# Kernel tuning notes

Hardware: AMD Instinct MI355X
Metric: run time of the kernel (lower is better)

Reference implementation:

```python
import jax, jax.numpy as jnp
import numpy as np

B, S, H, F, E, TOP_K = 2, 1024, 2048, 1408, 8, 2
SHARED_F = 2 * F  # moe_intermediate_size * n_shared_experts


def setup_inputs() -> dict:
    key = jax.random.key(0)
    ks = jax.random.split(key, 8)
    s = 0.02  # init scale for weights
    return {
        "hidden_states": jax.random.normal(ks[0], (B, S, H), jnp.float32),
        "gate_weight": jax.random.normal(ks[1], (E, H), jnp.float32) * s,
        "gate_proj": jax.random.normal(ks[2], (E, H, F), jnp.float32) * s,
        "up_proj": jax.random.normal(ks[3], (E, H, F), jnp.float32) * s,
        "down_proj": jax.random.normal(ks[4], (E, F, H), jnp.float32) * s,
        "shared_gate": jax.random.normal(ks[5], (H, SHARED_F), jnp.float32) * s,
        "shared_up": jax.random.normal(ks[6], (H, SHARED_F), jnp.float32) * s,
        "shared_down": jax.random.normal(ks[7], (SHARED_F, H), jnp.float32) * s,
    }


def reference(hidden_states, gate_weight, gate_proj, up_proj, down_proj,
              shared_gate, shared_up, shared_down):
    orig_shape = hidden_states.shape
    x = hidden_states.reshape(-1, orig_shape[-1])  # [T, H]
    T = x.shape[0]

    # MoEGate: softmax scores, top-k routing (no renorm)
    scores = jax.nn.softmax(x @ gate_weight.T, axis=-1)  # [T, E]
    topk_w, topk_idx = jax.lax.top_k(scores, TOP_K)      # [T, K]
    # dense combine weights: zero except selected experts
    combine = jnp.zeros_like(scores).at[jnp.arange(T)[:, None], topk_idx].set(topk_w)  # [T, E]

    # FusedSigmaMLP on all experts (math equal to sort/pad/grouped-GEMM/scatter-add path)
    gate_h = jnp.einsum('td,edf->etf', x, gate_proj)     # [E, T, F]
    up_h = jnp.einsum('td,edf->etf', x, up_proj)          # [E, T, F]
    expert_out = jnp.einsum('etf,efd->etd', jax.nn.silu(gate_h) * up_h, down_proj)  # [E, T, H]
    y = jnp.einsum('etd,te->td', expert_out, combine)     # weighted combine

    # shared experts (SigmaMLP with intermediate = moe_intermediate * n_shared)
    shared = (jax.nn.silu(x @ shared_gate) * (x @ shared_up)) @ shared_down
    return (y + shared).reshape(orig_shape)
```

## Files before the change

### kernel.cpp

```cpp
#include <hip/hip_runtime.h>
#include <hip/hip_bf16.h>

constexpr int T_ = 2048;
constexpr int H_ = 2048;
constexpr int F_ = 1408;
constexpr int E_ = 8;
constexpr int SF_ = 2816;

typedef __bf16 bf16;
typedef bf16 bf16x8 __attribute__((ext_vector_type(8)));
typedef float f32x4 __attribute__((ext_vector_type(4)));

#define DEVI __device__ __forceinline__

DEVI void async16(const void* g, void* l) {
    __builtin_amdgcn_global_load_lds(
        (const __attribute__((address_space(1))) unsigned int*)g,
        (__attribute__((address_space(3))) unsigned int*)l, 16, 0, 0);
}

__global__ void transpose_cvt(const float* __restrict__ src, bf16* __restrict__ dst,
                              int R, int C) {
    int z = blockIdx.z;
    src += (size_t)z * R * C;
    dst += (size_t)z * R * C;
    __shared__ float tile[32][33];
    int tx = threadIdx.x, ty = threadIdx.y;
    int c0 = blockIdx.x * 32, r0 = blockIdx.y * 32;
#pragma unroll
    for (int i = 0; i < 4; i++)
        tile[ty + i * 8][tx] = src[(size_t)(r0 + ty + i * 8) * C + c0 + tx];
    __syncthreads();
#pragma unroll
    for (int i = 0; i < 4; i++)
        dst[(size_t)(c0 + ty + i * 8) * R + r0 + tx] = (bf16)tile[tx][ty + i * 8];
}

__global__ void convert_x(const float* __restrict__ x, bf16* __restrict__ xb) {
    int i = (blockIdx.x * 256 + threadIdx.x) * 8;
    float4 a = *(const float4*)(x + i);
    float4 b = *(const float4*)(x + i + 4);
    bf16x8 v;
    v[0] = (bf16)a.x; v[1] = (bf16)a.y; v[2] = (bf16)a.z; v[3] = (bf16)a.w;
    v[4] = (bf16)b.x; v[5] = (bf16)b.y; v[6] = (bf16)b.z; v[7] = (bf16)b.w;
    *(bf16x8*)(xb + i) = v;
}

__global__ void gate_route(const float* __restrict__ x, const float* __restrict__ gw,
                           int* __restrict__ cnt, int* __restrict__ list,
                           float* __restrict__ wlist) {
    int t = blockIdx.x;
    int tid = threadIdx.x;
    float p[E_];
#pragma unroll
    for (int e = 0; e < E_; e++) p[e] = 0.f;
    const float* xr = x + (size_t)t * H_;
    for (int h = tid; h < H_; h += 256) {
        float xv = xr[h];
#pragma unroll
        for (int e = 0; e < E_; e++) p[e] += xv * gw[e * H_ + h];
    }
#pragma unroll
    for (int e = 0; e < E_; e++)
#pragma unroll
        for (int off = 32; off > 0; off >>= 1) p[e] += __shfl_down(p[e], off, 64);
    __shared__ float wred[4][E_];
    int lane = tid & 63, wid = tid >> 6;
    if (lane == 0)
#pragma unroll
        for (int e = 0; e < E_; e++) wred[wid][e] = p[e];
    __syncthreads();
    if (tid == 0) {
        float l[E_];
#pragma unroll
        for (int e = 0; e < E_; e++) l[e] = wred[0][e] + wred[1][e] + wred[2][e] + wred[3][e];
        float mx = l[0];
#pragma unroll
        for (int e = 1; e < E_; e++) mx = fmaxf(mx, l[e]);
        float sc[E_], s = 0.f;
#pragma unroll
        for (int e = 0; e < E_; e++) { sc[e] = __expf(l[e] - mx); s += sc[e]; }
#pragma unroll
        for (int e = 0; e < E_; e++) sc[e] /= s;
        int i1 = 0;
#pragma unroll
        for (int e = 1; e < E_; e++) if (sc[e] > sc[i1]) i1 = e;
        int i2 = (i1 == 0) ? 1 : 0;
#pragma unroll
        for (int e = 0; e < E_; e++) if (e != i1 && sc[e] > sc[i2]) i2 = e;
        int p1 = atomicAdd(&cnt[i1], 1);
        list[i1 * T_ + p1] = t; wlist[i1 * T_ + p1] = sc[i1];
        int p2 = atomicAdd(&cnt[i2], 1);
        list[i2 * T_ + p2] = t; wlist[i2 * T_ + p2] = sc[i2];
    }
}

__global__ void gather_rows(const bf16* __restrict__ xb, const int* __restrict__ cnt,
                            const int* __restrict__ list, bf16* __restrict__ xA) {
    int i = blockIdx.x, e = blockIdx.y;
    if (i >= cnt[e]) return;
    int t = list[e * T_ + i];
    const float4* s = (const float4*)(xb + (size_t)t * H_);
    float4* d = (float4*)(xA + ((size_t)e * T_ + i) * H_);
    d[threadIdx.x] = s[threadIdx.x];
}

__global__ void gemm_dual(const bf16* __restrict__ A, const bf16* __restrict__ Bg,
                          const bf16* __restrict__ Bu, bf16* __restrict__ Cact,
                          const int* __restrict__ cntPtr, int Mfull, int K, int N,
                          long sAe, long sBe, long sCe) {
    int e = blockIdx.z;
    A += (size_t)e * sAe; Bg += (size_t)e * sBe; Bu += (size_t)e * sBe;
    Cact += (size_t)e * sCe;
    int M = cntPtr ? cntPtr[e] : Mfull;
    int row0 = blockIdx.y * 128;
    if (row0 >= M) return;
    int col0 = blockIdx.x * 64;

    __shared__ __align__(16) bf16 As[128 * 64];
    __shared__ __align__(16) bf16 Bgs[64 * 64];
    __shared__ __align__(16) bf16 Bus[64 * 64];

    int tid = threadIdx.x, lane = tid & 63, wid = tid >> 6;
    int wm = (wid >> 1) * 64, wn = (wid & 1) * 32;
    int lm = lane & 15, lq = lane >> 4;

    f32x4 accg[4][2] = {};
    f32x4 accu[4][2] = {};

    int nkt = K >> 6;
    for (int kt = 0; kt < nkt; kt++) {
        int k0 = kt * 64;
#pragma unroll
        for (int j = 0; j < 4; j++) {
            int L = j * 256 + tid;
            int m = L >> 3, cp = L & 7, c = cp ^ (m & 7);
            int gr = row0 + m; if (gr >= M) gr = M - 1;
            async16(A + (size_t)gr * K + k0 + c * 8, (void*)(As + L * 8));
        }
#pragma unroll
        for (int j = 0; j < 2; j++) {
            int L = j * 256 + tid;
            int n = L >> 3, cp = L & 7, c = cp ^ (n & 7);
            async16(Bg + (size_t)(col0 + n) * K + k0 + c * 8, (void*)(Bgs + L * 8));
            async16(Bu + (size_t)(col0 + n) * K + k0 + c * 8, (void*)(Bus + L * 8));
        }
        __syncthreads();
#pragma unroll
        for (int kk = 0; kk < 2; kk++) {
            bf16x8 af[4], bgf[2], buf_[2];
            int cc = kk * 4 + lq;
#pragma unroll
            for (int mi = 0; mi < 4; mi++) {
                int r = wm + mi * 16 + lm;
                af[mi] = *(const bf16x8*)(As + r * 64 + ((cc ^ (r & 7)) * 8));
            }
#pragma unroll
            for (int ni = 0; ni < 2; ni++) {
                int r = wn + ni * 16 + lm;
                bgf[ni]  = *(const bf16x8*)(Bgs + r * 64 + ((cc ^ (r & 7)) * 8));
                buf_[ni] = *(const bf16x8*)(Bus + r * 64 + ((cc ^ (r & 7)) * 8));
            }
#pragma unroll
            for (int mi = 0; mi < 4; mi++)
#pragma unroll
                for (int ni = 0; ni < 2; ni++) {
                    accg[mi][ni] = __builtin_amdgcn_mfma_f32_16x16x32_bf16(af[mi], bgf[ni], accg[mi][ni], 0, 0, 0);
                    accu[mi][ni] = __builtin_amdgcn_mfma_f32_16x16x32_bf16(af[mi], buf_[ni], accu[mi][ni], 0, 0, 0);
                }
        }
        __syncthreads();
    }
#pragma unroll
    for (int mi = 0; mi < 4; mi++)
#pragma unroll
        for (int r = 0; r < 4; r++) {
            int gr = row0 + wm + mi * 16 + lq * 4 + r;
            if (gr >= M) continue;
#pragma unroll
            for (int ni = 0; ni < 2; ni++) {
                int gc = col0 + wn + ni * 16 + lm;
                float g = accg[mi][ni][r], u = accu[mi][ni][r];
                float act = g / (1.f + __expf(-g)) * u;
                Cact[(size_t)gr * N + gc] = (bf16)act;
            }
        }
}

__global__ void gemm_single(const bf16* __restrict__ A, const bf16* __restrict__ Bt,
                            float* __restrict__ Out, const int* __restrict__ cntPtr,
                            int Mfull, int K, int N, const int* __restrict__ list,
                            const float* __restrict__ wlist, long sAe, long sBe) {
    int e = blockIdx.z;
    A += (size_t)e * sAe; Bt += (size_t)e * sBe;
    const int* lst = list ? list + (size_t)e * T_ : nullptr;
    const float* wl = wlist ? wlist + (size_t)e * T_ : nullptr;
    int M = cntPtr ? cntPtr[e] : Mfull;
    int row0 = blockIdx.y * 128;
    if (row0 >= M) return;
    int col0 = blockIdx.x * 128;

    __shared__ __align__(16) bf16 As[128 * 64];
    __shared__ __align__(16) bf16 Bs[128 * 64];

    int tid = threadIdx.x, lane = tid & 63, wid = tid >> 6;
    int wm = (wid >> 1) * 64, wn = (wid & 1) * 64;
    int lm = lane & 15, lq = lane >> 4;

    f32x4 acc[4][4] = {};
    int nkt = K >> 6;
    for (int kt = 0; kt < nkt; kt++) {
        int k0 = kt * 64;
#pragma unroll
        for (int j = 0; j < 4; j++) {
            int L = j * 256 + tid;
            int m = L >> 3, cp = L & 7, c = cp ^ (m & 7);
            int gr = row0 + m; if (gr >= M) gr = M - 1;
            async16(A + (size_t)gr * K + k0 + c * 8, (void*)(As + L * 8));
            async16(Bt + (size_t)(col0 + m) * K + k0 + c * 8, (void*)(Bs + L * 8));
        }
        __syncthreads();
#pragma unroll
        for (int kk = 0; kk < 2; kk++) {
            bf16x8 af[4], bfr[4];
            int cc = kk * 4 + lq;
#pragma unroll
            for (int i = 0; i < 4; i++) {
                int ra = wm + i * 16 + lm;
                af[i] = *(const bf16x8*)(As + ra * 64 + ((cc ^ (ra & 7)) * 8));
                int rb = wn + i * 16 + lm;
                bfr[i] = *(const bf16x8*)(Bs + rb * 64 + ((cc ^ (rb & 7)) * 8));
            }
#pragma unroll
            for (int mi = 0; mi < 4; mi++)
#pragma unroll
                for (int ni = 0; ni < 4; ni++)
                    acc[mi][ni] = __builtin_amdgcn_mfma_f32_16x16x32_bf16(af[mi], bfr[ni], acc[mi][ni], 0, 0, 0);
        }
        __syncthreads();
    }
#pragma unroll
    for (int mi = 0; mi < 4; mi++)
#pragma unroll
        for (int r = 0; r < 4; r++) {
            int cr = row0 + wm + mi * 16 + lq * 4 + r;
            if (cr >= M) continue;
            if (lst) {
                int t = lst[cr];
                float w = wl[cr];
#pragma unroll
                for (int ni = 0; ni < 4; ni++) {
                    int gc = col0 + wn + ni * 16 + lm;
                    atomicAdd(&Out[(size_t)t * N + gc], w * acc[mi][ni][r]);
                }
            } else {
#pragma unroll
                for (int ni = 0; ni < 4; ni++) {
                    int gc = col0 + wn + ni * 16 + lm;
                    Out[(size_t)cr * N + gc] = acc[mi][ni][r];
                }
            }
        }
}

extern "C" void kernel_launch(void* const* d_in, const int* in_sizes, int n_in,
                              void* d_out, int out_size, void* d_ws, size_t ws_size,
                              hipStream_t stream) {
    const float* x     = (const float*)d_in[0];
    const float* gw    = (const float*)d_in[1];
    const float* gproj = (const float*)d_in[2];
    const float* uproj = (const float*)d_in[3];
    const float* dproj = (const float*)d_in[4];
    const float* sg    = (const float*)d_in[5];
    const float* su    = (const float*)d_in[6];
    const float* sd    = (const float*)d_in[7];
    float* out = (float*)d_out;

    char* w = (char*)d_ws;
    size_t off = 0;
    auto alloc = [&](size_t bytes) { void* p = w + off; off += (bytes + 255) & ~(size_t)255; return p; };
    bf16* wg_t   = (bf16*)alloc((size_t)E_ * F_ * H_ * 2);
    bf16* wu_t   = (bf16*)alloc((size_t)E_ * F_ * H_ * 2);
    bf16* wd_t   = (bf16*)alloc((size_t)E_ * H_ * F_ * 2);
    bf16* sg_t   = (bf16*)alloc((size_t)SF_ * H_ * 2);
    bf16* su_t   = (bf16*)alloc((size_t)SF_ * H_ * 2);
    bf16* sd_t   = (bf16*)alloc((size_t)H_ * SF_ * 2);
    bf16* xb     = (bf16*)alloc((size_t)T_ * H_ * 2);
    bf16* xA     = (bf16*)alloc((size_t)E_ * T_ * H_ * 2);
    bf16* act    = (bf16*)alloc((size_t)E_ * T_ * F_ * 2);
    bf16* act_sh = (bf16*)alloc((size_t)T_ * SF_ * 2);
    int*  cnt    = (int*)alloc(256);
    int*  list   = (int*)alloc((size_t)E_ * T_ * 4);
    float* wlist = (float*)alloc((size_t)E_ * T_ * 4);
    (void)ws_size; (void)in_sizes; (void)n_in; (void)out_size;

    hipMemsetAsync(cnt, 0, 256, stream);

    dim3 tb(32, 8);
    transpose_cvt<<<dim3(F_ / 32, H_ / 32, E_), tb, 0, stream>>>(gproj, wg_t, H_, F_);
    transpose_cvt<<<dim3(F_ / 32, H_ / 32, E_), tb, 0, stream>>>(uproj, wu_t, H_, F_);
    transpose_cvt<<<dim3(H_ / 32, F_ / 32, E_), tb, 0, stream>>>(dproj, wd_t, F_, H_);
    transpose_cvt<<<dim3(SF_ / 32, H_ / 32, 1), tb, 0, stream>>>(sg, sg_t, H_, SF_);
    transpose_cvt<<<dim3(SF_ / 32, H_ / 32, 1), tb, 0, stream>>>(su, su_t, H_, SF_);
    transpose_cvt<<<dim3(H_ / 32, SF_ / 32, 1), tb, 0, stream>>>(sd, sd_t, SF_, H_);

    convert_x<<<T_ * H_ / (256 * 8), 256, 0, stream>>>(x, xb);
    gate_route<<<T_, 256, 0, stream>>>(x, gw, cnt, list, wlist);
    gather_rows<<<dim3(T_, E_), 256, 0, stream>>>(xb, cnt, list, xA);

    gemm_dual<<<dim3(F_ / 64, T_ / 128, E_), 256, 0, stream>>>(
        xA, wg_t, wu_t, act, cnt, T_, H_, F_,
        (long)T_ * H_, (long)F_ * H_, (long)T_ * F_);
    gemm_dual<<<dim3(SF_ / 64, T_ / 128, 1), 256, 0, stream>>>(
        xb, sg_t, su_t, act_sh, nullptr, T_, H_, SF_, 0, 0, 0);
    gemm_single<<<dim3(H_ / 128, T_ / 128, 1), 256, 0, stream>>>(
        act_sh, sd_t, out, nullptr, T_, SF_, H_, nullptr, nullptr, 0, 0);
    gemm_single<<<dim3(H_ / 128, T_ / 128, E_), 256, 0, stream>>>(
        act, wd_t, out, cnt, T_, F_, H_, list, wlist,
        (long)T_ * F_, (long)H_ * F_);
}
```

Measured before the change: 678.7 us.

## Launch GEMMs as compact 1D grids with row-stride loops and XCD-aware block mapping

Replaces the 3D grids, where many expert row-blocks exited immediately because their token count was below the tile, with 1D grids. Each block loops over row tiles with a stride and skips the empty ones. Block IDs are decoded so consecutive IDs (id&7) map to different experts or column groups, which spreads work across XCDs and aims to improve L2 reuse of weight tiles. This reduces wasted block launches and balances load, at the cost of serial row loops per block, which can create tail imbalance when expert counts are uneven.

```diff
diff --git a/kernel.cpp b/kernel.cpp
--- a/kernel.cpp
+++ b/kernel.cpp
@@ -105,17 +105,24 @@
     d[threadIdx.x] = s[threadIdx.x];
 }
 
+template <bool EXP>
 __global__ void gemm_dual(const bf16* __restrict__ A, const bf16* __restrict__ Bg,
                           const bf16* __restrict__ Bu, bf16* __restrict__ Cact,
                           const int* __restrict__ cntPtr, int Mfull, int K, int N,
-                          long sAe, long sBe, long sCe) {
-    int e = blockIdx.z;
+                          long sAe, long sBe, long sCe, int ncol, int ncg, int RS) {
+    int id = blockIdx.x;
+    int e, col, rs;
+    if (EXP) {
+        e = id & 7; int r = id >> 3; col = r % ncol; rs = r / ncol;
+    } else {
+        e = 0; int c8 = id & 7; int r = id >> 3;
+        int cg = r % ncg; rs = r / ncg; col = cg * 8 + c8;
+        if (col >= ncol) return;
+    }
     A += (size_t)e * sAe; Bg += (size_t)e * sBe; Bu += (size_t)e * sBe;
     Cact += (size_t)e * sCe;
     int M = cntPtr ? cntPtr[e] : Mfull;
-    int row0 = blockIdx.y * 128;
-    if (row0 >= M) return;
-    int col0 = blockIdx.x * 64;
+    int col0 = col * 64;
 
     __shared__ __align__(16) bf16 As[128 * 64];
     __shared__ __align__(16) bf16 Bgs[64 * 64];
@@ -124,81 +131,92 @@
     int tid = threadIdx.x, lane = tid & 63, wid = tid >> 6;
     int wm = (wid >> 1) * 64, wn = (wid & 1) * 32;
     int lm = lane & 15, lq = lane >> 4;
-
-    f32x4 accg[4][2] = {};
-    f32x4 accu[4][2] = {};
-
     int nkt = K >> 6;
-    for (int kt = 0; kt < nkt; kt++) {
-        int k0 = kt * 64;
-#pragma unroll
-        for (int j = 0; j < 4; j++) {
-            int L = j * 256 + tid;
-            int m = L >> 3, cp = L & 7, c = cp ^ (m & 7);
-            int gr = row0 + m; if (gr >= M) gr = M - 1;
-            async16(A + (size_t)gr * K + k0 + c * 8, (void*)(As + L * 8));
+
+    for (int rb = rs; rb * 128 < M; rb += RS) {
+        int row0 = rb * 128;
+        f32x4 accg[4][2] = {};
+        f32x4 accu[4][2] = {};
+
+        for (int kt = 0; kt < nkt; kt++) {
+            int k0 = kt * 64;
+#pragma unroll
+            for (int j = 0; j < 4; j++) {
+                int L = j * 256 + tid;
+                int m = L >> 3, cp = L & 7, c = cp ^ (m & 7);
+                int gr = row0 + m; if (gr >= M) gr = M - 1;
+                async16(A + (size_t)gr * K + k0 + c * 8, (void*)(As + L * 8));
+            }
+#pragma unroll
+            for (int j = 0; j < 2; j++) {
+                int L = j * 256 + tid;
+                int n = L >> 3, cp = L & 7, c = cp ^ (n & 7);
+                async16(Bg + (size_t)(col0 + n) * K + k0 + c * 8, (void*)(Bgs + L * 8));
+                async16(Bu + (size_t)(col0 + n) * K + k0 + c * 8, (void*)(Bus + L * 8));
+            }
+            __syncthreads();
+#pragma unroll
+            for (int kk = 0; kk < 2; kk++) {
+                bf16x8 af[4], bgf[2], buf_[2];
+                int cc = kk * 4 + lq;
+#pragma unroll
+                for (int mi = 0; mi < 4; mi++) {
+                    int r = wm + mi * 16 + lm;
+                    af[mi] = *(const bf16x8*)(As + r * 64 + ((cc ^ (r & 7)) * 8));
+                }
+#pragma unroll
+                for (int ni = 0; ni < 2; ni++) {
+                    int r = wn + ni * 16 + lm;
+                    bgf[ni]  = *(const bf16x8*)(Bgs + r * 64 + ((cc ^ (r & 7)) * 8));
+                    buf_[ni] = *(const bf16x8*)(Bus + r * 64 + ((cc ^ (r & 7)) * 8));
+                }
+#pragma unroll
+                for (int mi = 0; mi < 4; mi++)
+#pragma unroll
+                    for (int ni = 0; ni < 2; ni++) {
+                        accg[mi][ni] = __builtin_amdgcn_mfma_f32_16x16x32_bf16(af[mi], bgf[ni], accg[mi][ni], 0, 0, 0);
+                        accu[mi][ni] = __builtin_amdgcn_mfma_f32_16x16x32_bf16(af[mi], buf_[ni], accu[mi][ni], 0, 0, 0);
+                    }
+            }
+            __syncthreads();
         }
 #pragma unroll
-        for (int j = 0; j < 2; j++) {
-            int L = j * 256 + tid;
-            int n = L >> 3, cp = L & 7, c = cp ^ (n & 7);
-            async16(Bg + (size_t)(col0 + n) * K + k0 + c * 8, (void*)(Bgs + L * 8));
-            async16(Bu + (size_t)(col0 + n) * K + k0 + c * 8, (void*)(Bus + L * 8));
-        }
-        __syncthreads();
-#pragma unroll
-        for (int kk = 0; kk < 2; kk++) {
-            bf16x8 af[4], bgf[2], buf_[2];
-            int cc = kk * 4 + lq;
-#pragma unroll
-            for (int mi = 0; mi < 4; mi++) {
-                int r = wm + mi * 16 + lm;
-                af[mi] = *(const bf16x8*)(As + r * 64 + ((cc ^ (r & 7)) * 8));
-            }
-#pragma unroll
-            for (int ni = 0; ni < 2; ni++) {
-                int r = wn + ni * 16 + lm;
-                bgf[ni]  = *(const bf16x8*)(Bgs + r * 64 + ((cc ^ (r & 7)) * 8));
-                buf_[ni] = *(const bf16x8*)(Bus + r * 64 + ((cc ^ (r & 7)) * 8));
-            }
-#pragma unroll
-            for (int mi = 0; mi < 4; mi++)
+        for (int mi = 0; mi < 4; mi++)
+#pragma unroll
+            for (int r = 0; r < 4; r++) {
+                int gr = row0 + wm + mi * 16 + lq * 4 + r;
+                if (gr >= M) continue;
 #pragma unroll
                 for (int ni = 0; ni < 2; ni++) {
-                    accg[mi][ni] = __builtin_amdgcn_mfma_f32_16x16x32_bf16(af[mi], bgf[ni], accg[mi][ni], 0, 0, 0);
-                    accu[mi][ni] = __builtin_amdgcn_mfma_f32_16x16x32_bf16(af[mi], buf_[ni], accu[mi][ni], 0, 0, 0);
-                }
-        }
-        __syncthreads();
-    }
-#pragma unroll
-    for (int mi = 0; mi < 4; mi++)
-#pragma unroll
-        for (int r = 0; r < 4; r++) {
-            int gr = row0 + wm + mi * 16 + lq * 4 + r;
-            if (gr >= M) continue;
-#pragma unroll
-            for (int ni = 0; ni < 2; ni++) {
-                int gc = col0 + wn + ni * 16 + lm;
-                float g = accg[mi][ni][r], u = accu[mi][ni][r];
-                float act = g / (1.f + __expf(-g)) * u;
-                Cact[(size_t)gr * N + gc] = (bf16)act;
-            }
-        }
-}
-
+                    int gc = col0 + wn + ni * 16 + lm;
+                    float g = accg[mi][ni][r], u = accu[mi][ni][r];
+                    float act = g / (1.f + __expf(-g)) * u;
+                    Cact[(size_t)gr * N + gc] = (bf16)act;
+                }
+            }
+    }
+}
+
+template <bool EXP>
 __global__ void gemm_single(const bf16* __restrict__ A, const bf16* __restrict__ Bt,
                             float* __restrict__ Out, const int* __restrict__ cntPtr,
                             int Mfull, int K, int N, const int* __restrict__ list,
-                            const float* __restrict__ wlist, long sAe, long sBe) {
-    int e = blockIdx.z;
+                            const float* __restrict__ wlist, long sAe, long sBe,
+                            int ncol, int ncg, int RS) {
+    int id = blockIdx.x;
+    int e, col, rs;
+    if (EXP) {
+        e = id & 7; int r = id >> 3; col = r % ncol; rs = r / ncol;
+    } else {
+        e = 0; int c8 = id & 7; int r = id >> 3;
+        int cg = r % ncg; rs = r / ncg; col = cg * 8 + c8;
+        if (col >= ncol) return;
+    }
     A += (size_t)e * sAe; Bt += (size_t)e * sBe;
     const int* lst = list ? list + (size_t)e * T_ : nullptr;
     const float* wl = wlist ? wlist + (size_t)e * T_ : nullptr;
     int M = cntPtr ? cntPtr[e] : Mfull;
-    int row0 = blockIdx.y * 128;
-    if (row0 >= M) return;
-    int col0 = blockIdx.x * 128;
+    int col0 = col * 128;
 
     __shared__ __align__(16) bf16 As[128 * 64];
     __shared__ __align__(16) bf16 Bs[128 * 64];
@@ -206,61 +224,65 @@
     int tid = threadIdx.x, lane = tid & 63, wid = tid >> 6;
     int wm = (wid >> 1) * 64, wn = (wid & 1) * 64;
     int lm = lane & 15, lq = lane >> 4;
-
-    f32x4 acc[4][4] = {};
     int nkt = K >> 6;
-    for (int kt = 0; kt < nkt; kt++) {
-        int k0 = kt * 64;
-#pragma unroll
-        for (int j = 0; j < 4; j++) {
-            int L = j * 256 + tid;
-            int m = L >> 3, cp = L & 7, c = cp ^ (m & 7);
-            int gr = row0 + m; if (gr >= M) gr = M - 1;
-            async16(A + (size_t)gr * K + k0 + c * 8, (void*)(As + L * 8));
-            async16(Bt + (size_t)(col0 + m) * K + k0 + c * 8, (void*)(Bs + L * 8));
+
+    for (int rb = rs; rb * 128 < M; rb += RS) {
+        int row0 = rb * 128;
+        f32x4 acc[4][4] = {};
+
+        for (int kt = 0; kt < nkt; kt++) {
+            int k0 = kt * 64;
+#pragma unroll
+            for (int j = 0; j < 4; j++) {
+                int L = j * 256 + tid;
+                int m = L >> 3, cp = L & 7, c = cp ^ (m & 7);
+                int gr = row0 + m; if (gr >= M) gr = M - 1;
+                async16(A + (size_t)gr * K + k0 + c * 8, (void*)(As + L * 8));
+                async16(Bt + (size_t)(col0 + m) * K + k0 + c * 8, (void*)(Bs + L * 8));
+            }
+            __syncthreads();
+#pragma unroll
+            for (int kk = 0; kk < 2; kk++) {
+                bf16x8 af[4], bfr[4];
+                int cc = kk * 4 + lq;
+#pragma unroll
+                for (int i = 0; i < 4; i++) {
+                    int ra = wm + i * 16 + lm;
+                    af[i] = *(const bf16x8*)(As + ra * 64 + ((cc ^ (ra & 7)) * 8));
+                    int rb2 = wn + i * 16 + lm;
+                    bfr[i] = *(const bf16x8*)(Bs + rb2 * 64 + ((cc ^ (rb2 & 7)) * 8));
+                }
+#pragma unroll
+                for (int mi = 0; mi < 4; mi++)
+#pragma unroll
+                    for (int ni = 0; ni < 4; ni++)
+                        acc[mi][ni] = __builtin_amdgcn_mfma_f32_16x16x32_bf16(af[mi], bfr[ni], acc[mi][ni], 0, 0, 0);
+            }
+            __syncthreads();
         }
-        __syncthreads();
-#pragma unroll
-        for (int kk = 0; kk < 2; kk++) {
-            bf16x8 af[4], bfr[4];
-            int cc = kk * 4 + lq;
-#pragma unroll
-            for (int i = 0; i < 4; i++) {
-                int ra = wm + i * 16 + lm;
-                af[i] = *(const bf16x8*)(As + ra * 64 + ((cc ^ (ra & 7)) * 8));
-                int rb = wn + i * 16 + lm;
-                bfr[i] = *(const bf16x8*)(Bs + rb * 64 + ((cc ^ (rb & 7)) * 8));
-            }
-#pragma unroll
-            for (int mi = 0; mi < 4; mi++)
-#pragma unroll
-                for (int ni = 0; ni < 4; ni++)
-                    acc[mi][ni] = __builtin_amdgcn_mfma_f32_16x16x32_bf16(af[mi], bfr[ni], acc[mi][ni], 0, 0, 0);
-        }
-        __syncthreads();
-    }
-#pragma unroll
-    for (int mi = 0; mi < 4; mi++)
-#pragma unroll
-        for (int r = 0; r < 4; r++) {
-            int cr = row0 + wm + mi * 16 + lq * 4 + r;
-            if (cr >= M) continue;
-            if (lst) {
-                int t = lst[cr];
-                float w = wl[cr];
-#pragma unroll
-                for (int ni = 0; ni < 4; ni++) {
-                    int gc = col0 + wn + ni * 16 + lm;
-                    atomicAdd(&Out[(size_t)t * N + gc], w * acc[mi][ni][r]);
-                }
-            } else {
-#pragma unroll
-                for (int ni = 0; ni < 4; ni++) {
-                    int gc = col0 + wn + ni * 16 + lm;
-                    Out[(size_t)cr * N + gc] = acc[mi][ni][r];
-                }
-            }
-        }
+#pragma unroll
+        for (int mi = 0; mi < 4; mi++)
+#pragma unroll
+            for (int r = 0; r < 4; r++) {
+                int cr = row0 + wm + mi * 16 + lq * 4 + r;
+                if (cr >= M) continue;
+                if (lst) {
+                    int t = lst[cr];
+                    float w = wl[cr];
+#pragma unroll
+                    for (int ni = 0; ni < 4; ni++) {
+                        int gc = col0 + wn + ni * 16 + lm;
+                        atomicAdd(&Out[(size_t)t * N + gc], w * acc[mi][ni][r]);
+                    }
+                } else {
+#pragma unroll
+                    for (int ni = 0; ni < 4; ni++) {
+                        int gc = col0 + wn + ni * 16 + lm;
+                        Out[(size_t)cr * N + gc] = acc[mi][ni][r];
+                    }
+                }
+            }
+    }
 }
 
 extern "C" void kernel_launch(void* const* d_in, const int* in_sizes, int n_in,
@@ -308,14 +330,14 @@
     gate_route<<<T_, 256, 0, stream>>>(x, gw, cnt, list, wlist);
     gather_rows<<<dim3(T_, E_), 256, 0, stream>>>(xb, cnt, list, xA);
 
-    gemm_dual<<<dim3(F_ / 64, T_ / 128, E_), 256, 0, stream>>>(
+    gemm_dual<true><<<8 * 22 * 4, 256, 0, stream>>>(
         xA, wg_t, wu_t, act, cnt, T_, H_, F_,
-        (long)T_ * H_, (long)F_ * H_, (long)T_ * F_);
-    gemm_dual<<<dim3(SF_ / 64, T_ / 128, 1), 256, 0, stream>>>(
-        xb, sg_t, su_t, act_sh, nullptr, T_, H_, SF_, 0, 0, 0);
-    gemm_single<<<dim3(H_ / 128, T_ / 128, 1), 256, 0, stream>>>(
-        act_sh, sd_t, out, nullptr, T_, SF_, H_, nullptr, nullptr, 0, 0);
-    gemm_single<<<dim3(H_ / 128, T_ / 128, E_), 256, 0, stream>>>(
+        (long)T_ * H_, (long)F_ * H_, (long)T_ * F_, 22, 0, 4);
+    gemm_dual<false><<<8 * 6 * 8, 256, 0, stream>>>(
+        xb, sg_t, su_t, act_sh, nullptr, T_, H_, SF_, 0, 0, 0, 44, 6, 8);
+    gemm_single<false><<<8 * 2 * 16, 256, 0, stream>>>(
+        act_sh, sd_t, out, nullptr, T_, SF_, H_, nullptr, nullptr, 0, 0, 16, 2, 16);
+    gemm_single<true><<<8 * 16 * 4, 256, 0, stream>>>(
         act, wd_t, out, cnt, T_, F_, H_, list, wlist,
-        (long)T_ * F_, (long)H_ * F_);
-}
+        (long)T_ * F_, (long)H_ * F_, 16, 0, 4);
+}
```

Measured after the change: 713.3 us. 1.05x slower.
